# Optimization experiments

Measured on AMD Instinct MI355X. Metric: run time of the kernel, lower is better.

The kernel has to match this reference:

```python
import jax, jax.numpy as jnp
import numpy as np

N, E, G, H, NF, EF, L = 50000, 800000, 512, 256, 32, 16, 4
BN_EPS = 1e-5


def setup_inputs() -> dict:
    key = jax.random.key(0)
    ks = iter(jax.random.split(key, 40))

    def W(shape, fan_in):
        return (jax.random.normal(next(ks), shape, jnp.float32) / np.sqrt(fan_in)).astype(jnp.float32)

    x = jax.random.normal(next(ks), (N, NF), jnp.float32)
    edge_index = jax.random.randint(next(ks), (2, E), 0, N)
    edge_attr = jax.random.normal(next(ks), (E, EF), jnp.float32)
    batch = jnp.sort(jax.random.randint(next(ks), (N,), 0, G))
    global_feat = jax.random.normal(next(ks), (G, NF), jnp.float32)

    inp = dict(x=x, edge_index=edge_index, edge_attr=edge_attr, batch=batch,
               global_feat=global_feat)
    # input projection
    inp['Win'] = W((NF, H), NF); inp['bin_'] = jnp.zeros((H,), jnp.float32)
    # per-layer GINEConv params (stacked over L layers)
    inp['We'] = W((L, EF, H), EF); inp['be'] = jnp.zeros((L, H), jnp.float32)
    inp['Wl1'] = W((L, H, H), H); inp['bl1'] = jnp.zeros((L, H), jnp.float32)
    inp['Wl2'] = W((L, H, H), H); inp['bl2'] = jnp.zeros((L, H), jnp.float32)
    # BatchNorm (eval mode: running stats)
    inp['bn_w'] = jnp.ones((L, H), jnp.float32); inp['bn_b'] = jnp.zeros((L, H), jnp.float32)
    inp['bn_m'] = jnp.zeros((L, H), jnp.float32); inp['bn_v'] = jnp.ones((L, H), jnp.float32)
    # projection head proj: H -> H//2 -> 64
    inp['Wp1'] = W((H, H // 2), H); inp['bp1'] = jnp.zeros((H // 2,), jnp.float32)
    inp['Wp2'] = W((H // 2, 64), H // 2); inp['bp2'] = jnp.zeros((64,), jnp.float32)
    # fc_final: (H+gfd) -> H -> H//2
    inp['Wf1'] = W((H + NF, H), H + NF); inp['bf1'] = jnp.zeros((H,), jnp.float32)
    inp['Wf2'] = W((H, H // 2), H); inp['bf2'] = jnp.zeros((H // 2,), jnp.float32)
    # edl head: H//2 -> 4
    inp['Whead'] = W((H // 2, 4), H // 2); inp['bhead'] = jnp.zeros((4,), jnp.float32)
    return inp


def reference(x, edge_index, edge_attr, batch, global_feat,
              Win, bin_, We, be, Wl1, bl1, Wl2, bl2,
              bn_w, bn_b, bn_m, bn_v,
              Wp1, bp1, Wp2, bp2, Wf1, bf1, Wf2, bf2, Whead, bhead):
    src, dst = edge_index[0], edge_index[1]
    h = x @ Win + bin_                                  # [N, H]
    for i in range(L):
        e = edge_attr @ We[i] + be[i]                   # [E, H] edge embedding
        msg = jax.nn.relu(h[src] + e)                   # GINEConv message
        aggr = jax.ops.segment_sum(msg, dst, num_segments=N)
        t = h + aggr                                    # (1+eps)*x + aggr, eps=0
        t = jax.nn.relu(t @ Wl1[i] + bl1[i]) @ Wl2[i] + bl2[i]
        t = (t - bn_m[i]) * (bn_w[i] / jnp.sqrt(bn_v[i] + BN_EPS)) + bn_b[i]
        h = h + jax.nn.relu(t)                          # residual
    g = jax.ops.segment_sum(h, batch, num_segments=G)   # global_add_pool [G, H]
    z = jax.nn.relu(g @ Wp1 + bp1) @ Wp2 + bp2          # [G, 64]
    z = z / jnp.maximum(jnp.linalg.norm(z, axis=1, keepdims=True), 1e-12)
    gc = jnp.concatenate([g, global_feat], axis=1)      # [G, H+gfd]
    gf = jax.nn.relu(jax.nn.relu(gc @ Wf1 + bf1) @ Wf2 + bf2)
    o = gf @ Whead + bhead                              # [G, 4]
    gamma = o[:, 0]
    nu = jax.nn.softplus(o[:, 1]) + 1e-6
    alpha = jax.nn.softplus(o[:, 2]) + 1.0 + 1e-6
    beta = jax.nn.softplus(o[:, 3]) + 1e-6
    edl = jnp.stack([gamma, nu, alpha, beta], axis=1)
    return edl, z, g
```

## Files before the change

### kernel.cpp

```cpp
#include <hip/hip_runtime.h>
#include <math.h>

#define N_NODES 50000
#define N_EDGES 800000
#define G_GRAPHS 512
#define H_DIM 256
#define NF_DIM 32
#define EF_DIM 16
#define L_LAYERS 4
#define BN_EPS 1e-5f

typedef __bf16 bf16_t;
typedef __attribute__((ext_vector_type(8))) __bf16 bf16x8;
typedef __attribute__((ext_vector_type(4))) float f32x4;
typedef _Float16 f16_t;
typedef __attribute__((ext_vector_type(2))) _Float16 f16x2;
typedef __attribute__((ext_vector_type(8))) _Float16 f16x8;

union f16x8_pairs {
  f16x8 v;
  f16x2 p[4];
};

__global__ __launch_bounds__(256) void k_init_h(
    const float* __restrict__ x, const float* __restrict__ Win,
    const float* __restrict__ bin, float* __restrict__ h,
    bf16_t* __restrict__ hb) {
  int row = blockIdx.x;
  int c = threadIdx.x;
  __shared__ float xs[NF_DIM];
  if (threadIdx.x < NF_DIM) xs[threadIdx.x] = x[(size_t)row * NF_DIM + threadIdx.x];
  __syncthreads();
  float acc = bin[c];
#pragma unroll
  for (int k = 0; k < NF_DIM; ++k) acc += xs[k] * Win[k * H_DIM + c];
  h[(size_t)row * H_DIM + c] = acc;
  hb[(size_t)row * H_DIM + c] = (bf16_t)acc;
}

__global__ __launch_bounds__(256) void k_prepW(
    const float* __restrict__ W, bf16_t* __restrict__ Wt) {
  int n = blockIdx.x;
  int l = blockIdx.y;
  int k = threadIdx.x;
  Wt[(size_t)l * 65536 + n * 256 + k] = (bf16_t)W[(size_t)l * 65536 + k * 256 + n];
}

__global__ __launch_bounds__(256) void k_deg(
    const int* __restrict__ dsts, int* __restrict__ deg) {
  int e = blockIdx.x * 256 + threadIdx.x;
  if (e < N_EDGES) atomicAdd(&deg[dsts[e]], 1);
}

#define SCAN_B 512
__global__ __launch_bounds__(SCAN_B) void k_scan1(
    const int* __restrict__ deg, int* __restrict__ incl, int* __restrict__ bsum) {
  __shared__ int s[SCAN_B];
  int gidx = blockIdx.x * SCAN_B + threadIdx.x;
  int v = (gidx < N_NODES) ? deg[gidx] : 0;
  s[threadIdx.x] = v;
  __syncthreads();
  for (int off = 1; off < SCAN_B; off <<= 1) {
    int t = (threadIdx.x >= off) ? s[threadIdx.x - off] : 0;
    __syncthreads();
    s[threadIdx.x] += t;
    __syncthreads();
  }
  if (gidx < N_NODES) incl[gidx] = s[threadIdx.x];
  if (threadIdx.x == SCAN_B - 1) bsum[blockIdx.x] = s[SCAN_B - 1];
}

__global__ void k_scan2(int* __restrict__ bsum, int nb) {
  if (threadIdx.x == 0 && blockIdx.x == 0) {
    int acc = 0;
    for (int i = 0; i < nb; ++i) { int t = bsum[i]; bsum[i] = acc; acc += t; }
  }
}

__global__ __launch_bounds__(SCAN_B) void k_scan3(
    const int* __restrict__ incl, const int* __restrict__ deg,
    const int* __restrict__ bsum, int* __restrict__ off) {
  int gidx = blockIdx.x * SCAN_B + threadIdx.x;
  if (gidx < N_NODES) off[gidx] = incl[gidx] - deg[gidx] + bsum[blockIdx.x];
  if (gidx == 0) off[N_NODES] = N_EDGES;
}

__global__ __launch_bounds__(256) void k_scatter(
    const int* __restrict__ srcs, const int* __restrict__ dsts,
    const int* __restrict__ off, int* __restrict__ fill,
    int* __restrict__ eid, int* __restrict__ src_csr) {
  int e = blockIdx.x * 256 + threadIdx.x;
  if (e < N_EDGES) {
    int d = dsts[e];
    int pos = atomicAdd(&fill[d], 1);
    int idx = off[d] + pos;
    eid[idx] = e;
    src_csr[idx] = srcs[e];
  }
}

__global__ __launch_bounds__(256) void k_gather_ea(
    const int* __restrict__ eid, const float* __restrict__ ea,
    f16_t* __restrict__ eac) {
  size_t idx = (size_t)blockIdx.x * 256 + threadIdx.x;
  int i = (int)(idx >> 4), k = (int)(idx & 15);
  eac[idx] = (f16_t)ea[(size_t)eid[i] * EF_DIM + k];
}

#define AGGR_GRID 12544

__device__ __forceinline__ void edge_dot2(const f16_t* __restrict__ eac,
                                          size_t i, const f16x2* __restrict__ w0,
                                          const f16x2* __restrict__ w1,
                                          float& m0, float& m1) {
  const f16x8* pp = (const f16x8*)(eac + i * EF_DIM);
  f16x8_pairs u0, u1;
  u0.v = pp[0];
  u1.v = pp[1];
#pragma unroll
  for (int j = 0; j < 4; ++j) {
    m0 = __builtin_amdgcn_fdot2(u0.p[j], w0[j], m0, false);
    m1 = __builtin_amdgcn_fdot2(u0.p[j], w1[j], m1, false);
  }
#pragma unroll
  for (int j = 0; j < 4; ++j) {
    m0 = __builtin_amdgcn_fdot2(u1.p[j], w0[j + 4], m0, false);
    m1 = __builtin_amdgcn_fdot2(u1.p[j], w1[j + 4], m1, false);
  }
}

__global__ __launch_bounds__(128) void k_aggr(
    const int* __restrict__ off, const int* __restrict__ src_csr,
    const f16_t* __restrict__ eac, const float* __restrict__ h,
    const bf16_t* __restrict__ hb, const float* __restrict__ We,
    const float* __restrict__ be, bf16_t* __restrict__ t0b) {
  const int tid = threadIdx.x;
  const int c0 = tid * 2;
  f16x2 w0[8], w1[8];
#pragma unroll
  for (int j = 0; j < 8; ++j) {
    f16x2 t0, t1;
    t0[0] = (f16_t)We[(2 * j) * H_DIM + c0];
    t0[1] = (f16_t)We[(2 * j + 1) * H_DIM + c0];
    t1[0] = (f16_t)We[(2 * j) * H_DIM + c0 + 1];
    t1[1] = (f16_t)We[(2 * j + 1) * H_DIM + c0 + 1];
    w0[j] = t0;
    w1[j] = t1;
  }
  const float be0 = be[c0], be1 = be[c0 + 1];
  const unsigned* __restrict__ hb32 = (const unsigned*)hb;
  for (int n = blockIdx.x; n < N_NODES; n += AGGR_GRID) {
    const int s0 = off[n], s1 = off[n + 1];
    float acc0 = 0.f, acc1 = 0.f;
    int i = s0;
    for (; i + 4 <= s1; i += 4) {
      int sA = src_csr[i], sB = src_csr[i + 1], sC = src_csr[i + 2], sD = src_csr[i + 3];
      unsigned uA = hb32[(unsigned)sA * 128u + tid];
      unsigned uB = hb32[(unsigned)sB * 128u + tid];
      unsigned uC = hb32[(unsigned)sC * 128u + tid];
      unsigned uD = hb32[(unsigned)sD * 128u + tid];
      float mA0 = be0, mA1 = be1, mB0 = be0, mB1 = be1;
      float mC0 = be0, mC1 = be1, mD0 = be0, mD1 = be1;
      edge_dot2(eac, (size_t)i, w0, w1, mA0, mA1);
      edge_dot2(eac, (size_t)i + 1, w0, w1, mB0, mB1);
      edge_dot2(eac, (size_t)i + 2, w0, w1, mC0, mC1);
      edge_dot2(eac, (size_t)i + 3, w0, w1, mD0, mD1);
      acc0 += fmaxf(mA0 + __uint_as_float(uA << 16), 0.f) +
              fmaxf(mB0 + __uint_as_float(uB << 16), 0.f) +
              fmaxf(mC0 + __uint_as_float(uC << 16), 0.f) +
              fmaxf(mD0 + __uint_as_float(uD << 16), 0.f);
      acc1 += fmaxf(mA1 + __uint_as_float(uA & 0xFFFF0000u), 0.f) +
              fmaxf(mB1 + __uint_as_float(uB & 0xFFFF0000u), 0.f) +
              fmaxf(mC1 + __uint_as_float(uC & 0xFFFF0000u), 0.f) +
              fmaxf(mD1 + __uint_as_float(uD & 0xFFFF0000u), 0.f);
    }
    for (; i < s1; ++i) {
      int s = src_csr[i];
      unsigned u = hb32[(unsigned)s * 128u + tid];
      float m0 = be0, m1 = be1;
      edge_dot2(eac, (size_t)i, w0, w1, m0, m1);
      acc0 += fmaxf(m0 + __uint_as_float(u << 16), 0.f);
      acc1 += fmaxf(m1 + __uint_as_float(u & 0xFFFF0000u), 0.f);
    }
    float2 hn = *(const float2*)&h[(size_t)n * H_DIM + c0];
    union { bf16_t b[2]; unsigned u; } pk;
    pk.b[0] = (bf16_t)(hn.x + acc0);
    pk.b[1] = (bf16_t)(hn.y + acc1);
    ((unsigned*)t0b)[(size_t)n * 128 + tid] = pk.u;
  }
}

#define FM 64
#define LSTR 40
#define T1STR 264

__global__ __launch_bounds__(512) void k_mlp(
    const bf16_t* __restrict__ t0b, const bf16_t* __restrict__ W1t,
    const bf16_t* __restrict__ W2t, const float* __restrict__ b1,
    const float* __restrict__ b2, const float* __restrict__ bnw,
    const float* __restrict__ bnb, const float* __restrict__ bnm,
    const float* __restrict__ bnv, float* __restrict__ h,
    bf16_t* __restrict__ hb) {
  __shared__ bf16_t As[2][FM * LSTR];
  __shared__ bf16_t T1[FM * T1STR];
  const int tid = threadIdx.x;
  const int bm = blockIdx.x * FM;
  const int lane = tid & 63;
  const int wv = tid >> 6;
  const int wm = (wv & 1) * 32;
  const int wn = (wv >> 1) * 64;
  const int l15 = lane & 15;
  const int kg = lane >> 4;
  const bool stager = tid < 256;
  const int arow = (tid & 255) >> 2, ach = (tid & 3) * 8;
  f32x4 acc[2][4];

#pragma unroll
  for (int m = 0; m < 2; ++m)
#pragma unroll
    for (int n = 0; n < 4; ++n) acc[m][n] = (f32x4){0.f, 0.f, 0.f, 0.f};
  if (stager) {
    int grow = bm + arow;
    f32x4 v = {0.f, 0.f, 0.f, 0.f};
    if (grow < N_NODES) v = *(const f32x4*)&t0b[(size_t)grow * H_DIM + ach];
    *(f32x4*)&As[0][arow * LSTR + ach] = v;
  }
  __syncthreads();
  int p = 0;
  for (int ks = 0; ks < 8; ++ks) {
    const int k0 = ks * 32;
    bf16x8 af[2], bfr[4];
#pragma unroll
    for (int m = 0; m < 2; ++m)
      af[m] = *(const bf16x8*)&As[p][(wm + m * 16 + l15) * LSTR + kg * 8];
    if (ks < 7 && stager) {
      int grow = bm + arow;
      f32x4 v = {0.f, 0.f, 0.f, 0.f};
      if (grow < N_NODES)
        v = *(const f32x4*)&t0b[(size_t)grow * H_DIM + k0 + 32 + ach];
      *(f32x4*)&As[p ^ 1][arow * LSTR + ach] = v;
    }
#pragma unroll
    for (int n = 0; n < 4; ++n)
      bfr[n] = *(const bf16x8*)&W1t[(size_t)(wn + n * 16 + l15) * H_DIM + k0 + kg * 8];
#pragma unroll
    for (int m = 0; m < 2; ++m)
#pragma unroll
      for (int n = 0; n < 4; ++n)
        acc[m][n] =
            __builtin_amdgcn_mfma_f32_16x16x32_bf16(af[m], bfr[n], acc[m][n], 0, 0, 0);
    __syncthreads();
    p ^= 1;
  }
#pragma unroll
  for (int m = 0; m < 2; ++m) {
    int rl0 = wm + m * 16 + kg * 4;
#pragma unroll
    for (int n = 0; n < 4; ++n) {
      int col = wn + n * 16 + l15;
      float bi = b1[col];
#pragma unroll
      for (int r = 0; r < 4; ++r)
        T1[(rl0 + r) * T1STR + col] = (bf16_t)fmaxf(acc[m][n][r] + bi, 0.f);
    }
  }
  __syncthreads();

#pragma unroll
  for (int m = 0; m < 2; ++m)
#pragma unroll
    for (int n = 0; n < 4; ++n) acc[m][n] = (f32x4){0.f, 0.f, 0.f, 0.f};
  for (int ks = 0; ks < 8; ++ks) {
    const int k0 = ks * 32;
    bf16x8 af[2], bfr[4];
#pragma unroll
    for (int m = 0; m < 2; ++m)
      af[m] = *(const bf16x8*)&T1[(wm + m * 16 + l15) * T1STR + k0 + kg * 8];
#pragma unroll
    for (int n = 0; n < 4; ++n)
      bfr[n] = *(const bf16x8*)&W2t[(size_t)(wn + n * 16 + l15) * H_DIM + k0 + kg * 8];
#pragma unroll
    for (int m = 0; m < 2; ++m)
#pragma unroll
      for (int n = 0; n < 4; ++n)
        acc[m][n] =
            __builtin_amdgcn_mfma_f32_16x16x32_bf16(af[m], bfr[n], acc[m][n], 0, 0, 0);
  }
#pragma unroll
  for (int m = 0; m < 2; ++m) {
    int row0 = bm + wm + m * 16 + kg * 4;
#pragma unroll
    for (int n = 0; n < 4; ++n) {
      int col = wn + n * 16 + l15;
      float bi = b2[col];
      float sc = bnw[col] * rsqrtf(bnv[col] + BN_EPS);
      float mu = bnm[col];
      float sb = bnb[col];
#pragma unroll
      for (int r = 0; r < 4; ++r) {
        int rr = row0 + r;
        if (rr < N_NODES) {
          float v = (acc[m][n][r] + bi - mu) * sc + sb;
          float* hp = &h[(size_t)rr * H_DIM + col];
          float nh = *hp + fmaxf(v, 0.f);
          *hp = nh;
          hb[(size_t)rr * H_DIM + col] = (bf16_t)nh;
        }
      }
    }
  }
}

__global__ __launch_bounds__(1024) void k_pool(
    const int* __restrict__ batch, const float* __restrict__ h,
    float* __restrict__ g, float* __restrict__ out_g) {
  int gid = blockIdx.x;
  int c = threadIdx.x & 255;
  int rl = threadIdx.x >> 8;
  int lo = 0, hi = N_NODES;
  while (lo < hi) { int mid = (lo + hi) >> 1; if (batch[mid] < gid) lo = mid + 1; else hi = mid; }
  int start = lo;
  int lo2 = start, hi2 = N_NODES;
  while (lo2 < hi2) { int mid = (lo2 + hi2) >> 1; if (batch[mid] < gid + 1) lo2 = mid + 1; else hi2 = mid; }
  int end = lo2;
  float acc = 0.f;
  for (int n = start + rl; n < end; n += 4) acc += h[(size_t)n * H_DIM + c];
  __shared__ float red[4][H_DIM];
  red[rl][c] = acc;
  __syncthreads();
  if (rl == 0) {
    float s = red[0][c] + red[1][c] + red[2][c] + red[3][c];
    g[(size_t)gid * H_DIM + c] = s;
    out_g[(size_t)gid * H_DIM + c] = s;
  }
}

__device__ __forceinline__ float softplusf(float x) {
  return fmaxf(x, 0.f) + log1pf(expf(-fabsf(x)));
}

__global__ __launch_bounds__(256) void k_tail(
    const float* __restrict__ g, const float* __restrict__ gf,
    const float* __restrict__ Wp1, const float* __restrict__ bp1,
    const float* __restrict__ Wp2, const float* __restrict__ bp2,
    const float* __restrict__ Wf1, const float* __restrict__ bf1,
    const float* __restrict__ Wf2, const float* __restrict__ bf2,
    const float* __restrict__ Wh, const float* __restrict__ bh,
    float* __restrict__ out) {
  int gid = blockIdx.x;
  int c = threadIdx.x;
  __shared__ float gc[H_DIM + NF_DIM];
  __shared__ float z1[128];
  __shared__ float q1[H_DIM];
  __shared__ float q2[128];
  gc[c] = g[(size_t)gid * H_DIM + c];
  if (c < NF_DIM) gc[H_DIM + c] = gf[(size_t)gid * NF_DIM + c];
  __syncthreads();
  float aq = bf1[c];
#pragma unroll 8
  for (int k = 0; k < H_DIM + NF_DIM; ++k) aq += gc[k] * Wf1[k * H_DIM + c];
  if (c < 128) {
    float a = bp1[c];
#pragma unroll 8
    for (int k = 0; k < H_DIM; ++k) a += gc[k] * Wp1[k * 128 + c];
    z1[c] = fmaxf(a, 0.f);
  }
  q1[c] = fmaxf(aq, 0.f);
  __syncthreads();
  if (c < 64) {
    float a = bp2[c];
#pragma unroll 8
    for (int k = 0; k < 128; ++k) a += z1[k] * Wp2[k * 64 + c];
    float ss = a * a;
#pragma unroll
    for (int o = 32; o; o >>= 1) ss += __shfl_xor(ss, o);
    float nrm = fmaxf(sqrtf(ss), 1e-12f);
    out[2048 + (size_t)gid * 64 + c] = a / nrm;
  }
  if (c < 128) {
    float a = bf2[c];
#pragma unroll 8
    for (int k = 0; k < H_DIM; ++k) a += q1[k] * Wf2[k * 128 + c];
    q2[c] = fmaxf(a, 0.f);
  }
  __syncthreads();
  if (c < 4) {
    float a = bh[c];
#pragma unroll 8
    for (int k = 0; k < 128; ++k) a += q2[k] * Wh[k * 4 + c];
    float v;
    if (c == 0) v = a;
    else if (c == 2) v = softplusf(a) + 1.f + 1e-6f;
    else v = softplusf(a) + 1e-6f;
    out[(size_t)gid * 4 + c] = v;
  }
}

extern "C" void kernel_launch(void* const* d_in, const int* in_sizes, int n_in,
                              void* d_out, int out_size, void* d_ws, size_t ws_size,
                              hipStream_t stream) {
  const float* x     = (const float*)d_in[0];
  const int*   ei    = (const int*)d_in[1];
  const float* ea    = (const float*)d_in[2];
  const int*   batch = (const int*)d_in[3];
  const float* gf    = (const float*)d_in[4];
  const float* Win   = (const float*)d_in[5];
  const float* bin   = (const float*)d_in[6];
  const float* We    = (const float*)d_in[7];
  const float* be    = (const float*)d_in[8];
  const float* Wl1   = (const float*)d_in[9];
  const float* bl1   = (const float*)d_in[10];
  const float* Wl2   = (const float*)d_in[11];
  const float* bl2   = (const float*)d_in[12];
  const float* bnw   = (const float*)d_in[13];
  const float* bnb   = (const float*)d_in[14];
  const float* bnm   = (const float*)d_in[15];
  const float* bnv   = (const float*)d_in[16];
  const float* Wp1   = (const float*)d_in[17];
  const float* bp1   = (const float*)d_in[18];
  const float* Wp2   = (const float*)d_in[19];
  const float* bp2   = (const float*)d_in[20];
  const float* Wf1   = (const float*)d_in[21];
  const float* bf1   = (const float*)d_in[22];
  const float* Wf2   = (const float*)d_in[23];
  const float* bf2   = (const float*)d_in[24];
  const float* Wh    = (const float*)d_in[25];
  const float* bh    = (const float*)d_in[26];
  float* out = (float*)d_out;

  const int* srcs = ei;
  const int* dsts = ei + N_EDGES;

  const size_t NH = (size_t)N_NODES * H_DIM;
  float* h   = (float*)d_ws;
  float* g   = h + NH;
  f16_t* eac = (f16_t*)(g + (size_t)G_GRAPHS * H_DIM);
  bf16_t* t0b = (bf16_t*)(eac + (size_t)N_EDGES * EF_DIM);
  bf16_t* hb  = t0b + NH;
  bf16_t* Wt1 = hb + NH;
  bf16_t* Wt2 = Wt1 + (size_t)L_LAYERS * 65536;
  int* deg  = (int*)(Wt2 + (size_t)L_LAYERS * 65536);
  int* fill = deg + N_NODES;
  int* incl = fill + N_NODES;
  int* off  = incl + N_NODES;
  int* bsum = off + N_NODES + 1;
  int* eid  = bsum + 128;
  int* src_csr = eid + N_EDGES;

  hipMemsetAsync(deg, 0, N_NODES * sizeof(int), stream);
  hipMemsetAsync(fill, 0, N_NODES * sizeof(int), stream);
  const int nscan = (N_NODES + SCAN_B - 1) / SCAN_B;
  k_deg<<<(N_EDGES + 255) / 256, 256, 0, stream>>>(dsts, deg);
  k_scan1<<<nscan, SCAN_B, 0, stream>>>(deg, incl, bsum);
  k_scan2<<<1, 64, 0, stream>>>(bsum, nscan);
  k_scan3<<<nscan, SCAN_B, 0, stream>>>(incl, deg, bsum, off);
  k_scatter<<<(N_EDGES + 255) / 256, 256, 0, stream>>>(srcs, dsts, off, fill, eid, src_csr);
  k_gather_ea<<<(int)(((size_t)N_EDGES * EF_DIM) / 256), 256, 0, stream>>>(eid, ea, eac);
  dim3 wgrid(256, L_LAYERS);
  k_prepW<<<wgrid, 256, 0, stream>>>(Wl1, Wt1);
  k_prepW<<<wgrid, 256, 0, stream>>>(Wl2, Wt2);
  k_init_h<<<N_NODES, 256, 0, stream>>>(x, Win, bin, h, hb);

  const int mlpg = (N_NODES + FM - 1) / FM;
  for (int l = 0; l < L_LAYERS; ++l) {
    k_aggr<<<AGGR_GRID, 128, 0, stream>>>(off, src_csr, eac, h, hb,
                                          We + (size_t)l * EF_DIM * H_DIM,
                                          be + l * H_DIM, t0b);
    k_mlp<<<mlpg, 512, 0, stream>>>(t0b, Wt1 + (size_t)l * 65536,
                                    Wt2 + (size_t)l * 65536, bl1 + l * H_DIM,
                                    bl2 + l * H_DIM, bnw + l * H_DIM,
                                    bnb + l * H_DIM, bnm + l * H_DIM,
                                    bnv + l * H_DIM, h, hb);
  }

  float* out_g = out + 2048 + (size_t)G_GRAPHS * 64;
  k_pool<<<G_GRAPHS, 1024, 0, stream>>>(batch, h, g, out_g);
  k_tail<<<G_GRAPHS, 256, 0, stream>>>(g, gf, Wp1, bp1, Wp2, bp2, Wf1, bf1,
                                       Wf2, bf2, Wh, bh, out);
}
```

Before: 990.2 us.

## Drop fp32 node state, keep bf16 residual only; fuse edge-attr gather into scatter

Removes the fp32 copy of the node features and keeps only the bf16 array, so the aggregation, MLP residual update and pooling all read and write 2-byte values. This cuts per-layer memory traffic. The edge-attribute reordering is fused into the CSR scatter kernel, which drops the eid array and one launch, and the two weight-transpose launches are merged into one. The cost is accuracy: the residual now accumulates in bf16 across layers, so rounding error grows with depth.

```diff
diff --git a/kernel.cpp b/kernel.cpp
--- a/kernel.cpp
+++ b/kernel.cpp
@@ -24,8 +24,7 @@
 
 __global__ __launch_bounds__(256) void k_init_h(
     const float* __restrict__ x, const float* __restrict__ Win,
-    const float* __restrict__ bin, float* __restrict__ h,
-    bf16_t* __restrict__ hb) {
+    const float* __restrict__ bin, bf16_t* __restrict__ hb) {
   int row = blockIdx.x;
   int c = threadIdx.x;
   __shared__ float xs[NF_DIM];
@@ -34,15 +33,18 @@
   float acc = bin[c];
 #pragma unroll
   for (int k = 0; k < NF_DIM; ++k) acc += xs[k] * Win[k * H_DIM + c];
-  h[(size_t)row * H_DIM + c] = acc;
   hb[(size_t)row * H_DIM + c] = (bf16_t)acc;
 }
 
 __global__ __launch_bounds__(256) void k_prepW(
-    const float* __restrict__ W, bf16_t* __restrict__ Wt) {
+    const float* __restrict__ Wl1, const float* __restrict__ Wl2,
+    bf16_t* __restrict__ Wt1, bf16_t* __restrict__ Wt2) {
   int n = blockIdx.x;
-  int l = blockIdx.y;
+  int ly = blockIdx.y;
   int k = threadIdx.x;
+  const float* W = (ly < L_LAYERS) ? Wl1 : Wl2;
+  bf16_t* Wt = (ly < L_LAYERS) ? Wt1 : Wt2;
+  int l = ly & 3;
   Wt[(size_t)l * 65536 + n * 256 + k] = (bf16_t)W[(size_t)l * 65536 + k * 256 + n];
 }
 
@@ -88,23 +90,25 @@
 __global__ __launch_bounds__(256) void k_scatter(
     const int* __restrict__ srcs, const int* __restrict__ dsts,
     const int* __restrict__ off, int* __restrict__ fill,
-    int* __restrict__ eid, int* __restrict__ src_csr) {
+    int* __restrict__ src_csr, const float* __restrict__ ea,
+    f16_t* __restrict__ eac) {
   int e = blockIdx.x * 256 + threadIdx.x;
   if (e < N_EDGES) {
     int d = dsts[e];
     int pos = atomicAdd(&fill[d], 1);
     int idx = off[d] + pos;
-    eid[idx] = e;
     src_csr[idx] = srcs[e];
-  }
-}
-
-__global__ __launch_bounds__(256) void k_gather_ea(
-    const int* __restrict__ eid, const float* __restrict__ ea,
-    f16_t* __restrict__ eac) {
-  size_t idx = (size_t)blockIdx.x * 256 + threadIdx.x;
-  int i = (int)(idx >> 4), k = (int)(idx & 15);
-  eac[idx] = (f16_t)ea[(size_t)eid[i] * EF_DIM + k];
+    const f32x4* p = (const f32x4*)(ea + (size_t)e * EF_DIM);
+    f32x4 v0 = p[0], v1 = p[1], v2 = p[2], v3 = p[3];
+    f16x8 o0, o1;
+    o0[0] = (f16_t)v0.x; o0[1] = (f16_t)v0.y; o0[2] = (f16_t)v0.z; o0[3] = (f16_t)v0.w;
+    o0[4] = (f16_t)v1.x; o0[5] = (f16_t)v1.y; o0[6] = (f16_t)v1.z; o0[7] = (f16_t)v1.w;
+    o1[0] = (f16_t)v2.x; o1[1] = (f16_t)v2.y; o1[2] = (f16_t)v2.z; o1[3] = (f16_t)v2.w;
+    o1[4] = (f16_t)v3.x; o1[5] = (f16_t)v3.y; o1[6] = (f16_t)v3.z; o1[7] = (f16_t)v3.w;
+    f16x8* dst = (f16x8*)(eac + (size_t)idx * EF_DIM);
+    dst[0] = o0;
+    dst[1] = o1;
+  }
 }
 
 #define AGGR_GRID 12544
@@ -131,9 +135,9 @@
 
 __global__ __launch_bounds__(128) void k_aggr(
     const int* __restrict__ off, const int* __restrict__ src_csr,
-    const f16_t* __restrict__ eac, const float* __restrict__ h,
-    const bf16_t* __restrict__ hb, const float* __restrict__ We,
-    const float* __restrict__ be, bf16_t* __restrict__ t0b) {
+    const f16_t* __restrict__ eac, const bf16_t* __restrict__ hb,
+    const float* __restrict__ We, const float* __restrict__ be,
+    bf16_t* __restrict__ t0b) {
   const int tid = threadIdx.x;
   const int c0 = tid * 2;
   f16x2 w0[8], w1[8];
@@ -182,10 +186,12 @@
       acc0 += fmaxf(m0 + __uint_as_float(u << 16), 0.f);
       acc1 += fmaxf(m1 + __uint_as_float(u & 0xFFFF0000u), 0.f);
     }
-    float2 hn = *(const float2*)&h[(size_t)n * H_DIM + c0];
+    unsigned hu = hb32[(size_t)n * 128 + tid];
+    float h0 = __uint_as_float(hu << 16);
+    float h1 = __uint_as_float(hu & 0xFFFF0000u);
     union { bf16_t b[2]; unsigned u; } pk;
-    pk.b[0] = (bf16_t)(hn.x + acc0);
-    pk.b[1] = (bf16_t)(hn.y + acc1);
+    pk.b[0] = (bf16_t)(h0 + acc0);
+    pk.b[1] = (bf16_t)(h1 + acc1);
     ((unsigned*)t0b)[(size_t)n * 128 + tid] = pk.u;
   }
 }
@@ -199,8 +205,7 @@
     const bf16_t* __restrict__ W2t, const float* __restrict__ b1,
     const float* __restrict__ b2, const float* __restrict__ bnw,
     const float* __restrict__ bnb, const float* __restrict__ bnm,
-    const float* __restrict__ bnv, float* __restrict__ h,
-    bf16_t* __restrict__ hb) {
+    const float* __restrict__ bnv, bf16_t* __restrict__ hb) {
   __shared__ bf16_t As[2][FM * LSTR];
   __shared__ bf16_t T1[FM * T1STR];
   const int tid = threadIdx.x;
@@ -301,37 +306,45 @@
         int rr = row0 + r;
         if (rr < N_NODES) {
           float v = (acc[m][n][r] + bi - mu) * sc + sb;
-          float* hp = &h[(size_t)rr * H_DIM + col];
-          float nh = *hp + fmaxf(v, 0.f);
-          *hp = nh;
-          hb[(size_t)rr * H_DIM + col] = (bf16_t)nh;
+          size_t o = (size_t)rr * H_DIM + col;
+          float old = (float)hb[o];
+          hb[o] = (bf16_t)(old + fmaxf(v, 0.f));
         }
       }
     }
   }
 }
 
-__global__ __launch_bounds__(1024) void k_pool(
-    const int* __restrict__ batch, const float* __restrict__ h,
+__global__ __launch_bounds__(512) void k_pool(
+    const int* __restrict__ batch, const bf16_t* __restrict__ hb,
     float* __restrict__ g, float* __restrict__ out_g) {
   int gid = blockIdx.x;
-  int c = threadIdx.x & 255;
-  int rl = threadIdx.x >> 8;
+  int cp = threadIdx.x & 127;
+  int rl = threadIdx.x >> 7;
   int lo = 0, hi = N_NODES;
   while (lo < hi) { int mid = (lo + hi) >> 1; if (batch[mid] < gid) lo = mid + 1; else hi = mid; }
   int start = lo;
   int lo2 = start, hi2 = N_NODES;
   while (lo2 < hi2) { int mid = (lo2 + hi2) >> 1; if (batch[mid] < gid + 1) lo2 = mid + 1; else hi2 = mid; }
   int end = lo2;
-  float acc = 0.f;
-  for (int n = start + rl; n < end; n += 4) acc += h[(size_t)n * H_DIM + c];
+  const unsigned* hb32 = (const unsigned*)hb;
+  float a0 = 0.f, a1 = 0.f;
+  for (int n = start + rl; n < end; n += 4) {
+    unsigned u = hb32[(size_t)n * 128 + cp];
+    a0 += __uint_as_float(u << 16);
+    a1 += __uint_as_float(u & 0xFFFF0000u);
+  }
   __shared__ float red[4][H_DIM];
-  red[rl][c] = acc;
+  red[rl][2 * cp] = a0;
+  red[rl][2 * cp + 1] = a1;
   __syncthreads();
   if (rl == 0) {
-    float s = red[0][c] + red[1][c] + red[2][c] + red[3][c];
-    g[(size_t)gid * H_DIM + c] = s;
-    out_g[(size_t)gid * H_DIM + c] = s;
+    float s0 = red[0][2 * cp] + red[1][2 * cp] + red[2][2 * cp] + red[3][2 * cp];
+    float s1 = red[0][2 * cp + 1] + red[1][2 * cp + 1] + red[2][2 * cp + 1] + red[3][2 * cp + 1];
+    g[(size_t)gid * H_DIM + 2 * cp] = s0;
+    g[(size_t)gid * H_DIM + 2 * cp + 1] = s1;
+    out_g[(size_t)gid * H_DIM + 2 * cp] = s0;
+    out_g[(size_t)gid * H_DIM + 2 * cp + 1] = s1;
   }
 }
 
@@ -432,8 +445,7 @@
   const int* dsts = ei + N_EDGES;
 
   const size_t NH = (size_t)N_NODES * H_DIM;
-  float* h   = (float*)d_ws;
-  float* g   = h + NH;
+  float* g   = (float*)d_ws;
   f16_t* eac = (f16_t*)(g + (size_t)G_GRAPHS * H_DIM);
   bf16_t* t0b = (bf16_t*)(eac + (size_t)N_EDGES * EF_DIM);
   bf16_t* hb  = t0b + NH;
@@ -444,8 +456,7 @@
   int* incl = fill + N_NODES;
   int* off  = incl + N_NODES;
   int* bsum = off + N_NODES + 1;
-  int* eid  = bsum + 128;
-  int* src_csr = eid + N_EDGES;
+  int* src_csr = bsum + 128;
 
   hipMemsetAsync(deg, 0, N_NODES * sizeof(int), stream);
   hipMemsetAsync(fill, 0, N_NODES * sizeof(int), stream);
@@ -454,27 +465,26 @@
   k_scan1<<<nscan, SCAN_B, 0, stream>>>(deg, incl, bsum);
   k_scan2<<<1, 64, 0, stream>>>(bsum, nscan);
   k_scan3<<<nscan, SCAN_B, 0, stream>>>(incl, deg, bsum, off);
-  k_scatter<<<(N_EDGES + 255) / 256, 256, 0, stream>>>(srcs, dsts, off, fill, eid, src_csr);
-  k_gather_ea<<<(int)(((size_t)N_EDGES * EF_DIM) / 256), 256, 0, stream>>>(eid, ea, eac);
-  dim3 wgrid(256, L_LAYERS);
-  k_prepW<<<wgrid, 256, 0, stream>>>(Wl1, Wt1);
-  k_prepW<<<wgrid, 256, 0, stream>>>(Wl2, Wt2);
-  k_init_h<<<N_NODES, 256, 0, stream>>>(x, Win, bin, h, hb);
+  k_scatter<<<(N_EDGES + 255) / 256, 256, 0, stream>>>(srcs, dsts, off, fill,
+                                                       src_csr, ea, eac);
+  dim3 wgrid(256, 2 * L_LAYERS);
+  k_prepW<<<wgrid, 256, 0, stream>>>(Wl1, Wl2, Wt1, Wt2);
+  k_init_h<<<N_NODES, 256, 0, stream>>>(x, Win, bin, hb);
 
   const int mlpg = (N_NODES + FM - 1) / FM;
   for (int l = 0; l < L_LAYERS; ++l) {
-    k_aggr<<<AGGR_GRID, 128, 0, stream>>>(off, src_csr, eac, h, hb,
+    k_aggr<<<AGGR_GRID, 128, 0, stream>>>(off, src_csr, eac, hb,
                                           We + (size_t)l * EF_DIM * H_DIM,
                                           be + l * H_DIM, t0b);
     k_mlp<<<mlpg, 512, 0, stream>>>(t0b, Wt1 + (size_t)l * 65536,
                                     Wt2 + (size_t)l * 65536, bl1 + l * H_DIM,
                                     bl2 + l * H_DIM, bnw + l * H_DIM,
                                     bnb + l * H_DIM, bnm + l * H_DIM,
-                                    bnv + l * H_DIM, h, hb);
+                                    bnv + l * H_DIM, hb);
   }
 
   float* out_g = out + 2048 + (size_t)G_GRAPHS * 64;
-  k_pool<<<G_GRAPHS, 1024, 0, stream>>>(batch, h, g, out_g);
+  k_pool<<<G_GRAPHS, 512, 0, stream>>>(batch, hb, g, out_g);
   k_tail<<<G_GRAPHS, 256, 0, stream>>>(g, gf, Wp1, bp1, Wp2, bp2, Wf1, bf1,
                                        Wf2, bf2, Wh, bh, out);
 }
```

Result: faster. 899.3 us (-9.2%).
